# Kernel tuning notes

Hardware: AMD Instinct MI355X
Metric: run time of the kernel (lower is better)

Reference implementation:

```python
import jax, jax.numpy as jnp
import numpy as np

B, C_IN, H, W = 4, 256, 48, 48
HEADS, HD = 8, 64
N = H * W
SCALE = 1.0 / (HD ** 0.5)


def setup_inputs() -> dict:
    key = jax.random.key(0)
    ks = jax.random.split(key, 5)
    x = jax.random.normal(ks[0], (B, C_IN, H, W), dtype=jnp.float32)
    # 1x1 conv weights, squeezed: [heads, head_channels, in_channels]
    Wq = jax.random.normal(ks[1], (HEADS, HD, C_IN), dtype=jnp.float32) * (C_IN ** -0.5)
    Wk = jax.random.normal(ks[2], (HEADS, HD, C_IN), dtype=jnp.float32) * (C_IN ** -0.5)
    Wv = jax.random.normal(ks[3], (HEADS, HD, C_IN), dtype=jnp.float32) * (C_IN ** -0.5)
    # output 1x1 conv: [in_channels, heads*head_channels]
    Wo = jax.random.normal(ks[4], (C_IN, HEADS * HD), dtype=jnp.float32) * ((HEADS * HD) ** -0.5)
    return {"x": x, "Wq": Wq, "Wk": Wk, "Wv": Wv, "Wo": Wo}


def reference(x, Wq, Wk, Wv, Wo):
    b, c, h, w = x.shape
    n = h * w
    xf = x.reshape(b, c, n)  # [B, C, N]
    # per-head 1x1 convs == batched projections -> [heads, B, N, HD]
    q = jnp.einsum('hdc,bcn->hbnd', Wq, xf)
    k = jnp.einsum('hdc,bcn->hbnd', Wk, xf)
    v = jnp.einsum('hdc,bcn->hbnd', Wv, xf)
    scores = jnp.einsum('hbnd,hbmd->hbnm', q, k) * SCALE  # [heads, B, N, N]
    probs = jax.nn.softmax(scores, axis=-1)
    ws = jnp.einsum('hbnm,hbmd->hbnd', probs, v)  # [heads, B, N, HD]
    # faithful replication of torch: transpose(1,2) then reshape(B, heads*HD, H, W)
    ws = jnp.transpose(ws, (0, 2, 1, 3))  # [heads, N, B, HD]
    ws = ws.reshape(b, HEADS * HD, h, w)
    out = jnp.einsum('oc,bchw->bohw', Wo, ws)  # output 1x1 conv
    return out
```

## Files before the change

### kernel.cpp

```cpp
#include <hip/hip_runtime.h>

#define B_     4
#define CIN    256
#define NTOK   2304
#define HEADS  8
#define HD     64
#define SCALE  0.125f
#define LOG2E  1.44269504088896f
#define QSCALE (SCALE * LOG2E)
#define PBIAS  8.0f
#define QKV_ELEMS (HEADS * B_ * NTOK * HD)
#define HBSTRIDE 147456
#define WSZ    131072

typedef _Float16 f16;
typedef _Float16 __attribute__((ext_vector_type(8))) h8v;
typedef _Float16 __attribute__((ext_vector_type(4))) h4v;
typedef ushort   __attribute__((ext_vector_type(8))) us8;
typedef float    __attribute__((ext_vector_type(16))) f16v;

__device__ inline uint pk2(float a, float b) {
    auto v = __builtin_amdgcn_cvt_pkrtz(a, b);
    return __builtin_bit_cast(uint, v);
}
#define EXP2(x) __builtin_amdgcn_exp2f(x)

#define GLOAD_LDS(g, l) __builtin_amdgcn_global_load_lds( \
    (const __attribute__((address_space(1))) unsigned int*)(g), \
    (__attribute__((address_space(3))) unsigned int*)(l), 16, 0, 0)

__global__ __launch_bounds__(256) void castw(
    const float* __restrict__ Wq, const float* __restrict__ Wk,
    const float* __restrict__ Wv, const float* __restrict__ Wo,
    f16* __restrict__ wc, f16* __restrict__ woc)
{
    int e4 = (blockIdx.x * 256 + threadIdx.x) * 4;
    const float* src; f16* dst; float mult = 1.0f; int off;
    if (e4 < WSZ)          { src = Wq; off = e4;           dst = wc;           mult = QSCALE; }
    else if (e4 < 2 * WSZ) { src = Wk; off = e4 - WSZ;     dst = wc + WSZ; }
    else if (e4 < 3 * WSZ) { src = Wv; off = e4 - 2 * WSZ; dst = wc + 2 * WSZ; }
    else                   { src = Wo; off = e4 - 3 * WSZ; dst = woc; }
    float4 r = *(const float4*)(src + off);
    h4v hv;
    hv.x = (f16)(r.x * mult); hv.y = (f16)(r.y * mult);
    hv.z = (f16)(r.z * mult); hv.w = (f16)(r.w * mult);
    *(h4v*)(dst + off) = hv;
}

__global__ __launch_bounds__(256) void tcastf(
    const float* __restrict__ src, f16* __restrict__ dst, int C)
{
    const int n0 = blockIdx.x * 64;
    const int c0 = blockIdx.y * 64;
    const int b  = blockIdx.z;
    __shared__ float T[64][65];
    const int tid = threadIdx.x;
    const float* sb = src + ((size_t)b * C + c0) * NTOK;
    #pragma unroll
    for (int i = 0; i < 16; ++i) {
        int idx = tid + 256 * i;
        int rr = idx >> 6, ll = idx & 63;
        T[ll][rr] = sb[(size_t)rr * NTOK + n0 + ll];
    }
    __syncthreads();
    const size_t ob = ((size_t)b * NTOK + n0) * C + c0;
    #pragma unroll
    for (int i = 0; i < 4; ++i) {
        int idx = tid + 256 * i;
        int row = idx >> 4, c4 = (idx & 15) * 4;
        h4v v;
        v.x = (f16)T[row][c4 + 0]; v.y = (f16)T[row][c4 + 1];
        v.z = (f16)T[row][c4 + 2]; v.w = (f16)T[row][c4 + 3];
        *(h4v*)(dst + ob + (size_t)row * C + c4) = v;
    }
}

__global__ __launch_bounds__(128) void proj_mfma(
    const f16* __restrict__ wc, const f16* __restrict__ xt,
    f16* __restrict__ qh, f16* __restrict__ kh, f16* __restrict__ vth)
{
    const int ntile = blockIdx.x;
    const int hp    = blockIdx.y;
    const int b     = blockIdx.z;
    const int p     = hp >> 3, h = hp & 7;
    const int hb    = h * 4 + b;
    const f16* Wp = wc + ((size_t)p * 8 + h) * (HD * CIN);

    __shared__ __align__(16) f16 Ws[2][64][64], Xs[2][64][64];

    const int tid = threadIdx.x;
    const int w = tid >> 6, lane = tid & 63;
    const int lm = lane & 31, lh = lane >> 5;
    const int n_loc  = w * 32 + lm;
    const int n_glob = ntile * 64 + n_loc;

    const f16* xb = xt + ((size_t)b * NTOK + ntile * 64) * CIN;

    auto stage = [&](int buf, int c0) {
        const f16* src = (w == 0) ? Wp : xb;
        f16* dst = (w == 0) ? &Ws[buf][0][0] : &Xs[buf][0][0];
        #pragma unroll
        for (int i = 0; i < 8; ++i) {
            int g = i * 64 + lane; int row = g >> 3; int c = (g & 7) ^ (row & 7);
            GLOAD_LDS(src + (size_t)row * CIN + c0 + c * 8, dst + i * 512);
        }
    };

    f16v o0, o1;
    #pragma unroll
    for (int i = 0; i < 16; ++i) { o0[i] = 0.f; o1[i] = 0.f; }

    stage(0, 0);
    for (int c0 = 0; c0 < CIN; c0 += 64) {
        const int cur = (c0 >> 6) & 1;
        __syncthreads();
        if (c0 + 64 < CIN) stage(cur ^ 1, c0 + 64);
        #pragma unroll
        for (int s = 0; s < 4; ++s) {
            const int pp = ((2 * s + lh) ^ (lm & 7)) * 8;
            h8v a0 = *(const h8v*)&Ws[cur][lm][pp];
            h8v a1 = *(const h8v*)&Ws[cur][lm + 32][pp];
            h8v bh = *(const h8v*)&Xs[cur][n_loc][pp];
            o0 = __builtin_amdgcn_mfma_f32_32x32x16_f16(a0, bh, o0, 0, 0, 0);
            o1 = __builtin_amdgcn_mfma_f32_32x32x16_f16(a1, bh, o1, 0, 0, 0);
        }
    }

    const size_t hboff = (size_t)hb * HBSTRIDE;
    if (p < 2) {
        f16* oh = ((p == 0) ? qh : kh) + hboff + (size_t)n_glob * 64;
        #pragma unroll
        for (int t = 0; t < 2; ++t) {
            const f16v& oc = t ? o1 : o0;
            #pragma unroll
            for (int g = 0; g < 4; ++g) {
                int d0 = 8 * g + 4 * lh + 32 * t;
                h4v hv;
                hv.x = (f16)oc[4 * g + 0]; hv.y = (f16)oc[4 * g + 1];
                hv.z = (f16)oc[4 * g + 2]; hv.w = (f16)oc[4 * g + 3];
                *(h4v*)(oh + d0) = hv;
            }
        }
    } else {
        f16* oh = vth + hboff;
        #pragma unroll
        for (int t = 0; t < 2; ++t) {
            const f16v& oc = t ? o1 : o0;
            #pragma unroll
            for (int r = 0; r < 16; ++r) {
                int d = (r & 3) + 8 * (r >> 2) + 4 * lh + 32 * t;
                oh[(size_t)d * NTOK + n_glob] = (f16)oc[r];
            }
        }
    }
}

__global__ __launch_bounds__(256, 3) void attn_mfma(
    const f16* __restrict__ qh, const f16* __restrict__ kh,
    const f16* __restrict__ vth, f16* __restrict__ wsth)
{
    const int bid   = blockIdx.x;
    const int xcd   = bid & 7;
    const int slot  = bid >> 3;
    const int hb    = xcd * 4 + (slot / 36);
    const int rtile = slot % 36;
    const int h_    = hb >> 2, b = hb & 3;
    const int tid   = threadIdx.x;
    const int w     = tid >> 6;
    const int lane  = tid & 63;
    const int lm    = lane & 31;
    const int lh    = lane >> 5;
    const int rh    = w & 1;
    const int ks    = w >> 1;

    __shared__ __align__(16) f16 SMEM[2][2][64][64];

    const size_t hboff = (size_t)hb * HBSTRIDE;
    const int m = rtile * 64 + rh * 32 + lm;

    h8v Qf[4];
    #pragma unroll
    for (int s = 0; s < 4; ++s)
        Qf[s] = *(const h8v*)(qh + hboff + (size_t)m * 64 + (2 * s + lh) * 8);

    f16v o0, o1;
    #pragma unroll
    for (int i = 0; i < 16; ++i) { o0[i] = 0.f; o1[i] = 0.f; }
    float lsum = 0.f;

    const int  sv  = w >> 1;
    const int  stp = w & 1;
    const f16* gb  = (sv == 0) ? kh + hboff : vth + hboff;
    f16* lbase     = &SMEM[sv][stp][0][0];

    for (int st = 0; st < 18; ++st) {
        const int kts = 2 * st + stp;
        #pragma unroll
        for (int i = 0; i < 8; ++i) {
            int g   = i * 64 + lane;
            int row = g >> 3;
            int c   = (g & 7) ^ (row & 7);
            const f16* src = (sv == 0)
                ? gb + kts * 4096 + row * 64 + c * 8
                : gb + row * 2304 + kts * 64 + c * 8;
            *(uint4*)(lbase + g * 8) = *(const uint4*)src;
        }
        __syncthreads();

        f16v s0, s1;
        #pragma unroll
        for (int i = 0; i < 16; ++i) { s0[i] = 0.f; s1[i] = 0.f; }
        #pragma unroll
        for (int s = 0; s < 4; ++s) {
            const int p = ((2 * s + lh) ^ (lm & 7)) * 8;
            h8v k0 = *(const h8v*)&SMEM[0][ks][lm][p];
            h8v k1 = *(const h8v*)&SMEM[0][ks][lm + 32][p];
            s0 = __builtin_amdgcn_mfma_f32_32x32x16_f16(k0, Qf[s], s0, 0, 0, 0);
            s1 = __builtin_amdgcn_mfma_f32_32x32x16_f16(k1, Qf[s], s1, 0, 0, 0);
        }

        float rs = 0.f;
        #pragma unroll
        for (int i = 0; i < 16; ++i) { s0[i] = EXP2(s0[i] - PBIAS); rs += s0[i]; }
        #pragma unroll
        for (int i = 0; i < 16; ++i) { s1[i] = EXP2(s1[i] - PBIAS); rs += s1[i]; }
        lsum += rs;

        uint Ppk[2][8];
        #pragma unroll
        for (int pr = 0; pr < 8; ++pr) {
            Ppk[0][pr] = pk2(s0[2 * pr], s0[2 * pr + 1]);
            Ppk[1][pr] = pk2(s1[2 * pr], s1[2 * pr + 1]);
        }

        h8v pf[4];
        #pragma unroll
        for (int s = 0; s < 4; ++s) {
            const int jt = s >> 1, q = 4 * (s & 1);
            uint kp0 = lh ? Ppk[jt][q + 2] : Ppk[jt][q + 0];
            uint kp1 = lh ? Ppk[jt][q + 3] : Ppk[jt][q + 1];
            uint sp0 = lh ? Ppk[jt][q + 0] : Ppk[jt][q + 2];
            uint sp1 = lh ? Ppk[jt][q + 1] : Ppk[jt][q + 3];
            uint rp0 = (uint)__shfl_xor((int)sp0, 32);
            uint rp1 = (uint)__shfl_xor((int)sp1, 32);
            uint4 u = { lh ? rp0 : kp0, lh ? rp1 : kp1,
                        lh ? kp0 : rp0, lh ? kp1 : rp1 };
            pf[s] = __builtin_bit_cast(h8v, u);
        }

        #pragma unroll
        for (int s = 0; s < 4; ++s) {
            const int p = ((2 * s + lh) ^ (lm & 7)) * 8;
            h8v v0 = *(const h8v*)&SMEM[1][ks][lm][p];
            h8v v1 = *(const h8v*)&SMEM[1][ks][lm + 32][p];
            o0 = __builtin_amdgcn_mfma_f32_32x32x16_f16(v0, pf[s], o0, 0, 0, 0);
            o1 = __builtin_amdgcn_mfma_f32_32x32x16_f16(v1, pf[s], o1, 0, 0, 0);
        }
        __syncthreads();
    }

    float* red = (float*)&SMEM[0][0][0][0];
    if (ks == 1) {
        float* dst = red + (size_t)(rh * 64 + lane) * 33;
        #pragma unroll
        for (int i = 0; i < 16; ++i) { dst[i] = o0[i]; dst[16 + i] = o1[i]; }
        dst[32] = lsum;
    }
    __syncthreads();
    if (ks == 0) {
        const float* sp = red + (size_t)(rh * 64 + lane) * 33;
        #pragma unroll
        for (int i = 0; i < 16; ++i) { o0[i] += sp[i]; o1[i] += sp[16 + i]; }
        lsum += sp[32];
        lsum += __shfl_xor(lsum, 32);
        float inv = 1.0f / lsum;
        f16* wrow = wsth + ((size_t)h_ * NTOK + m) * 256 + b * 64;
        #pragma unroll
        for (int g = 0; g < 4; ++g) {
            h4v r0, r1;
            r0.x = (f16)(o0[4 * g + 0] * inv); r0.y = (f16)(o0[4 * g + 1] * inv);
            r0.z = (f16)(o0[4 * g + 2] * inv); r0.w = (f16)(o0[4 * g + 3] * inv);
            *(h4v*)(wrow + 8 * g + 4 * lh) = r0;
            r1.x = (f16)(o1[4 * g + 0] * inv); r1.y = (f16)(o1[4 * g + 1] * inv);
            r1.z = (f16)(o1[4 * g + 2] * inv); r1.w = (f16)(o1[4 * g + 3] * inv);
            *(h4v*)(wrow + 32 + 8 * g + 4 * lh) = r1;
        }
    }
}

__global__ __launch_bounds__(128) void outconv_mfma(
    const f16* __restrict__ woc, const f16* __restrict__ ws,
    float* __restrict__ out)
{
    const int ntile = blockIdx.x;
    const int otile = blockIdx.y;
    const int b     = blockIdx.z;

    __shared__ __align__(16) f16 Wos[2][64][64];
    __shared__ __align__(16) f16 Xs[2][64][72];

    const int tid = threadIdx.x;
    const int w = tid >> 6, lane = tid & 63;
    const int lm = lane & 31, lh = lane >> 5;
    const int n_loc  = w * 32 + lm;
    const int n_glob = ntile * 64 + n_loc;
    const int pr = tid >> 2;
    const int qn = tid & 3;

    const f16* Wb = woc + (size_t)(otile * 64) * 512;
    const f16* wsb = ws + (size_t)b * 512 * NTOK + ntile * 64 + qn * 16;

    auto stageW = [&](int buf, int c0) {
        #pragma unroll
        for (int j = 0; j < 4; ++j) {
            int i = w * 4 + j;
            int g = i * 64 + lane; int row = g >> 3; int c = (g & 7) ^ (row & 7);
            GLOAD_LDS(Wb + (size_t)row * 512 + c0 + c * 8,
                      &Wos[buf][0][0] + i * 512);
        }
    };

    uint4 x0, x1, x2, x3;
    auto loadB = [&](int c0) {
        const f16* r0 = wsb + (size_t)(c0 + 2 * pr) * NTOK;
        const f16* r1 = r0 + NTOK;
        x0 = *(const uint4*)(r0);
        x1 = *(const uint4*)(r0 + 8);
        x2 = *(const uint4*)(r1);
        x3 = *(const uint4*)(r1 + 8);
    };
    auto storeB = [&](int buf) {
        us8 a0 = __builtin_bit_cast(us8, x0), a1 = __builtin_bit_cast(us8, x1);
        us8 b0 = __builtin_bit_cast(us8, x2), b1 = __builtin_bit_cast(us8, x3);
        #pragma unroll
        for (int j = 0; j < 8; ++j) {
            *(uint*)&Xs[buf][qn * 16 + j][2 * pr]     = (uint)a0[j] | ((uint)b0[j] << 16);
            *(uint*)&Xs[buf][qn * 16 + 8 + j][2 * pr] = (uint)a1[j] | ((uint)b1[j] << 16);
        }
    };

    f16v o0, o1;
    #pragma unroll
    for (int i = 0; i < 16; ++i) { o0[i] = 0.f; o1[i] = 0.f; }

    stageW(0, 0);
    loadB(0);
    storeB(0);
    for (int c0 = 0; c0 < 512; c0 += 64) {
        const int cur = (c0 >> 6) & 1;
        __syncthreads();
        if (c0 + 64 < 512) { stageW(cur ^ 1, c0 + 64); loadB(c0 + 64); }
        #pragma unroll
        for (int s = 0; s < 4; ++s) {
            const int pp = ((2 * s + lh) ^ (lm & 7)) * 8;
            const int co = (2 * s + lh) * 8;
            h8v a0 = *(const h8v*)&Wos[cur][lm][pp];
            h8v a1 = *(const h8v*)&Wos[cur][lm + 32][pp];
            h8v bh = *(const h8v*)&Xs[cur][n_loc][co];
            o0 = __builtin_amdgcn_mfma_f32_32x32x16_f16(a0, bh, o0, 0, 0, 0);
            o1 = __builtin_amdgcn_mfma_f32_32x32x16_f16(a1, bh, o1, 0, 0, 0);
        }
        if (c0 + 64 < 512) storeB(cur ^ 1);
    }

    #pragma unroll
    for (int t = 0; t < 2; ++t) {
        const f16v& oc = t ? o1 : o0;
        #pragma unroll
        for (int r = 0; r < 16; ++r) {
            int orow = otile * 64 + (r & 3) + 8 * (r >> 2) + 4 * lh + 32 * t;
            out[((size_t)b * CIN + orow) * NTOK + n_glob] = oc[r];
        }
    }
}

extern "C" void kernel_launch(void* const* d_in, const int* in_sizes, int n_in,
                              void* d_out, int out_size, void* d_ws, size_t ws_size,
                              hipStream_t stream)
{
    const float* x  = (const float*)d_in[0];
    const float* Wq = (const float*)d_in[1];
    const float* Wk = (const float*)d_in[2];
    const float* Wv = (const float*)d_in[3];
    const float* Wo = (const float*)d_in[4];
    float* out = (float*)d_out;

    f16* qh   = (f16*)d_ws;
    f16* kh   = qh   + QKV_ELEMS;
    f16* vth  = kh   + QKV_ELEMS;
    f16* wsth = vth  + QKV_ELEMS;
    f16* xt   = wsth;
    f16* wc   = wsth + QKV_ELEMS;
    f16* woc  = wc   + 3 * WSZ;

    castw<<<dim3(512), 256, 0, stream>>>(Wq, Wk, Wv, Wo, wc, woc);
    tcastf<<<dim3(36, 4, 4), 256, 0, stream>>>(x, xt, CIN);
    proj_mfma<<<dim3(36, 24, 4), 128, 0, stream>>>(wc, xt, qh, kh, vth);
    attn_mfma<<<dim3(1152), 256, 0, stream>>>(qh, kh, vth, wsth);
    outconv_mfma<<<dim3(36, 4, 4), 128, 0, stream>>>(woc, wsth, out);
}
```

Baseline: 188.7 us.

## Split attention KV loop across four waves with private LDS tiles

Reworks the attention kernel so each block handles 32 query rows and each of its four waves walks its own slice of key/value tiles, staging them in a wave-private padded LDS buffer. This removes the two __syncthreads per KV step and halves per-block query work, doubling the grid. Occupancy hint rises to 4 blocks per CU. In exchange, each K/V tile is loaded from global memory by twice as many blocks, the tiles are smaller per MFMA, and the final reduction now merges three partial accumulators through LDS.

```diff
diff --git a/kernel.cpp b/kernel.cpp
--- a/kernel.cpp
+++ b/kernel.cpp
@@ -155,28 +155,29 @@
     }
 }
 
-__global__ __launch_bounds__(256, 3) void attn_mfma(
+__global__ __launch_bounds__(256, 4) void attn_mfma(
     const f16* __restrict__ qh, const f16* __restrict__ kh,
     const f16* __restrict__ vth, f16* __restrict__ wsth)
 {
     const int bid   = blockIdx.x;
     const int xcd   = bid & 7;
     const int slot  = bid >> 3;
-    const int hb    = xcd * 4 + (slot / 36);
-    const int rtile = slot % 36;
+    const int hb    = xcd * 4 + (slot / 72);
+    const int rtile = slot % 72;
     const int h_    = hb >> 2, b = hb & 3;
     const int tid   = threadIdx.x;
     const int w     = tid >> 6;
     const int lane  = tid & 63;
     const int lm    = lane & 31;
     const int lh    = lane >> 5;
-    const int rh    = w & 1;
-    const int ks    = w >> 1;
-
-    __shared__ __align__(16) f16 SMEM[2][2][64][64];
+
+    __shared__ __align__(16) unsigned char SMRAW[18432 + 20480];
+    f16* myK = (f16*)SMRAW + (size_t)w * (32 * 72);
+    f16* myV = (f16*)(SMRAW + 18432) + (size_t)w * (64 * 40);
+    float* red = (float*)SMRAW;
 
     const size_t hboff = (size_t)hb * HBSTRIDE;
-    const int m = rtile * 64 + rh * 32 + lm;
+    const int m = rtile * 32 + lm;
 
     h8v Qf[4];
     #pragma unroll
@@ -188,59 +189,53 @@
     for (int i = 0; i < 16; ++i) { o0[i] = 0.f; o1[i] = 0.f; }
     float lsum = 0.f;
 
-    const int  sv  = w >> 1;
-    const int  stp = w & 1;
-    const f16* gb  = (sv == 0) ? kh + hboff : vth + hboff;
-    f16* lbase     = &SMEM[sv][stp][0][0];
-
-    for (int st = 0; st < 18; ++st) {
-        const int kts = 2 * st + stp;
-        #pragma unroll
-        for (int i = 0; i < 8; ++i) {
-            int g   = i * 64 + lane;
-            int row = g >> 3;
-            int c   = (g & 7) ^ (row & 7);
-            const f16* src = (sv == 0)
-                ? gb + kts * 4096 + row * 64 + c * 8
-                : gb + row * 2304 + kts * 64 + c * 8;
-            *(uint4*)(lbase + g * 8) = *(const uint4*)src;
-        }
-        __syncthreads();
-
-        f16v s0, s1;
-        #pragma unroll
-        for (int i = 0; i < 16; ++i) { s0[i] = 0.f; s1[i] = 0.f; }
+    const f16* kb = kh + hboff;
+    const f16* vb = vth + hboff;
+
+    for (int t = 0; t < 18; ++t) {
+        const int jt = t * 4 + w;
+
+        #pragma unroll
+        for (int i = 0; i < 4; ++i) {
+            int g = i * 64 + lane;
+            int row = g >> 3, c = g & 7;
+            *(uint4*)(myK + row * 72 + c * 8) =
+                *(const uint4*)(kb + (size_t)(jt * 32 + row) * 64 + c * 8);
+        }
+        #pragma unroll
+        for (int i = 0; i < 4; ++i) {
+            int g = i * 64 + lane;
+            int row = g >> 2, c = g & 3;
+            *(uint4*)(myV + row * 40 + c * 8) =
+                *(const uint4*)(vb + (size_t)row * NTOK + jt * 32 + c * 8);
+        }
+
+        f16v s0;
+        #pragma unroll
+        for (int i = 0; i < 16; ++i) s0[i] = 0.f;
         #pragma unroll
         for (int s = 0; s < 4; ++s) {
-            const int p = ((2 * s + lh) ^ (lm & 7)) * 8;
-            h8v k0 = *(const h8v*)&SMEM[0][ks][lm][p];
-            h8v k1 = *(const h8v*)&SMEM[0][ks][lm + 32][p];
+            h8v k0 = *(const h8v*)(myK + lm * 72 + (2 * s + lh) * 8);
             s0 = __builtin_amdgcn_mfma_f32_32x32x16_f16(k0, Qf[s], s0, 0, 0, 0);
-            s1 = __builtin_amdgcn_mfma_f32_32x32x16_f16(k1, Qf[s], s1, 0, 0, 0);
         }
 
         float rs = 0.f;
         #pragma unroll
         for (int i = 0; i < 16; ++i) { s0[i] = EXP2(s0[i] - PBIAS); rs += s0[i]; }
-        #pragma unroll
-        for (int i = 0; i < 16; ++i) { s1[i] = EXP2(s1[i] - PBIAS); rs += s1[i]; }
         lsum += rs;
 
-        uint Ppk[2][8];
-        #pragma unroll
-        for (int pr = 0; pr < 8; ++pr) {
-            Ppk[0][pr] = pk2(s0[2 * pr], s0[2 * pr + 1]);
-            Ppk[1][pr] = pk2(s1[2 * pr], s1[2 * pr + 1]);
-        }
-
-        h8v pf[4];
-        #pragma unroll
-        for (int s = 0; s < 4; ++s) {
-            const int jt = s >> 1, q = 4 * (s & 1);
-            uint kp0 = lh ? Ppk[jt][q + 2] : Ppk[jt][q + 0];
-            uint kp1 = lh ? Ppk[jt][q + 3] : Ppk[jt][q + 1];
-            uint sp0 = lh ? Ppk[jt][q + 0] : Ppk[jt][q + 2];
-            uint sp1 = lh ? Ppk[jt][q + 1] : Ppk[jt][q + 3];
+        uint Ppk[8];
+        #pragma unroll
+        for (int pr = 0; pr < 8; ++pr) Ppk[pr] = pk2(s0[2 * pr], s0[2 * pr + 1]);
+
+        h8v pf[2];
+        #pragma unroll
+        for (int s = 0; s < 2; ++s) {
+            const int q = 4 * s;
+            uint kp0 = lh ? Ppk[q + 2] : Ppk[q + 0];
+            uint kp1 = lh ? Ppk[q + 3] : Ppk[q + 1];
+            uint sp0 = lh ? Ppk[q + 0] : Ppk[q + 2];
+            uint sp1 = lh ? Ppk[q + 1] : Ppk[q + 3];
             uint rp0 = (uint)__shfl_xor((int)sp0, 32);
             uint rp1 = (uint)__shfl_xor((int)sp1, 32);
             uint4 u = { lh ? rp0 : kp0, lh ? rp1 : kp1,
@@ -249,29 +244,30 @@
         }
 
         #pragma unroll
-        for (int s = 0; s < 4; ++s) {
-            const int p = ((2 * s + lh) ^ (lm & 7)) * 8;
-            h8v v0 = *(const h8v*)&SMEM[1][ks][lm][p];
-            h8v v1 = *(const h8v*)&SMEM[1][ks][lm + 32][p];
+        for (int s = 0; s < 2; ++s) {
+            h8v v0 = *(const h8v*)(myV + lm * 40 + (2 * s + lh) * 8);
+            h8v v1 = *(const h8v*)(myV + (lm + 32) * 40 + (2 * s + lh) * 8);
             o0 = __builtin_amdgcn_mfma_f32_32x32x16_f16(v0, pf[s], o0, 0, 0, 0);
             o1 = __builtin_amdgcn_mfma_f32_32x32x16_f16(v1, pf[s], o1, 0, 0, 0);
         }
-        __syncthreads();
-    }
-
-    float* red = (float*)&SMEM[0][0][0][0];
-    if (ks == 1) {
-        float* dst = red + (size_t)(rh * 64 + lane) * 33;
+    }
+
+    __syncthreads();
+    if (w != 0) {
+        float* dst = red + (size_t)((w - 1) * 64 + lane) * 33;
         #pragma unroll
         for (int i = 0; i < 16; ++i) { dst[i] = o0[i]; dst[16 + i] = o1[i]; }
         dst[32] = lsum;
     }
     __syncthreads();
-    if (ks == 0) {
-        const float* sp = red + (size_t)(rh * 64 + lane) * 33;
-        #pragma unroll
-        for (int i = 0; i < 16; ++i) { o0[i] += sp[i]; o1[i] += sp[16 + i]; }
-        lsum += sp[32];
+    if (w == 0) {
+        #pragma unroll
+        for (int pw = 0; pw < 3; ++pw) {
+            const float* sp = red + (size_t)(pw * 64 + lane) * 33;
+            #pragma unroll
+            for (int i = 0; i < 16; ++i) { o0[i] += sp[i]; o1[i] += sp[16 + i]; }
+            lsum += sp[32];
+        }
         lsum += __shfl_xor(lsum, 32);
         float inv = 1.0f / lsum;
         f16* wrow = wsth + ((size_t)h_ * NTOK + m) * 256 + b * 64;
@@ -396,6 +392,6 @@
     castw<<<dim3(512), 256, 0, stream>>>(Wq, Wk, Wv, Wo, wc, woc);
     tcastf<<<dim3(36, 4, 4), 256, 0, stream>>>(x, xt, CIN);
     proj_mfma<<<dim3(36, 24, 4), 128, 0, stream>>>(wc, xt, qh, kh, vth);
-    attn_mfma<<<dim3(1152), 256, 0, stream>>>(qh, kh, vth, wsth);
+    attn_mfma<<<dim3(2304), 256, 0, stream>>>(qh, kh, vth, wsth);
     outconv_mfma<<<dim3(36, 4, 4), 128, 0, stream>>>(woc, wsth, out);
 }
```

New measurement: 189.5 us. No clear change (+0.4%).
